# Performance work log

Measured on AMD Instinct MI355X. Metric: run time of the kernel, lower is better.

The kernel has to match this reference:

```python
import jax, jax.numpy as jnp
import numpy as np
import math

N_NODES = 4096
DEG = 32
N_EDGES = N_NODES * DEG
H = 128
NUM_NODE_STATES = 4
NUM_EDGE_STATES = 4
NUM_GRAPHS = 64
UPPER_T, LOWER_T, NUM_ITERS, TEMP_EVAL = 1.0, 0.1, 10000, 0.1
TRAINING_STEP = 1000
NEG_INF = -1.0e9


def temp_by_step(step):
    # linear anneal upper->lower over NUM_ITERS; eval temp when step == -1
    if step == -1:
        return TEMP_EVAL
    frac = min(step / float(NUM_ITERS), 1.0)
    return UPPER_T + (LOWER_T - UPPER_T) * frac


def from_binary_states(bits):
    w = 2 ** jnp.arange(bits.shape[-1], dtype=jnp.int32)
    return jnp.sum(bits.astype(jnp.int32) * w, axis=-1)


def group_argmax_onehot(vals, group, num_segments):
    # gumbel_softmax(vals, group, tau=0, use_noise=False): one-hot argmax per group
    seg_max = jax.ops.segment_max(vals, group, num_segments=num_segments)
    return (vals >= seg_max[group]).astype(jnp.int32)


def layernorm(x, g, b, eps=1e-5):
    mu = jnp.mean(x, -1, keepdims=True)
    var = jnp.mean((x - mu) ** 2, -1, keepdims=True)
    return (x - mu) * jax.lax.rsqrt(var + eps) * g + b


def select_best(emb, bits, scalars, index, num_index):
    states = 2 * from_binary_states(bits)                  # even state codes
    group = states * num_index + index.astype(jnp.int32)   # unique (state, index) id
    best = group_argmax_onehot(-scalars[:, 0], group, emb.shape[0] * num_index)
    return emb[states + best]


def _forward(node_states, edge_states, scalars, edge_index, batch_vec,
             reverse_idx, edge_pos, training_step,
             emb_virtual, emb_reciever, emb_edge, emb_static,
             w_q, w_k, w_v, w_ek, w_ev, w_comb,
             ln_q_g, ln_q_b, ln_k_g, ln_k_b,
             tg_w1, tg_b1, tg_w2, tg_b2):
    src, dst = edge_index[0], edge_index[1]
    N = node_states.shape[0]
    E = src.shape[0]
    D = E // N  # uniform in-degree (incl. self loop)
    h = w_q.shape[0]

    # per-node scalars come from the self-loop edges (exactly one per node)
    loop_vals = jnp.where((src == dst)[:, None], scalars, 0.0)
    node_scalars = jax.ops.segment_sum(loop_vals, dst, num_segments=N)  # [N,1]

    node_fts = select_best(emb_virtual, node_states, node_scalars, batch_vec, NUM_GRAPHS)
    edge_fts = emb_edge[from_binary_states(edge_states)]

    Q = layernorm(node_fts @ w_q.T, ln_q_g, ln_q_b)
    K = layernorm(node_fts @ w_k.T, ln_k_g, ln_k_b)
    V = node_fts @ w_v.T

    # combined edge K/V
    sb = select_best(emb_reciever, node_states[src], scalars, dst, N)
    sender_s = node_scalars[src]
    reciever_s = node_scalars[dst]
    rlx = (scalars < reciever_s).astype(jnp.int32)
    rlx_d = ((sender_s + scalars) < reciever_s).astype(jnp.int32)
    static_fts = emb_static[(rlx + 2 * rlx_d)[:, 0]]
    combined = jnp.concatenate([edge_fts, edge_fts[reverse_idx], static_fts], axis=-1) @ w_comb.T
    edge_K = sb @ w_ek.T
    edge_V = combined @ w_ev.T

    # dense ragged batch per destination node (to_dense_batch equivalent)
    Kc = K[src] + edge_K
    Vc = V[src] + edge_V
    dense_K = jnp.zeros((N, D, h), Kc.dtype).at[dst, edge_pos].set(Kc)
    dense_V = jnp.zeros((N, D, h), Vc.dtype).at[dst, edge_pos].set(Vc)
    mask = jnp.zeros((N, D), bool).at[dst, edge_pos].set(True)

    logits = jnp.einsum('nh,ndh->nd', Q, dense_K) / math.sqrt(h)
    logits = jnp.where(mask, logits, NEG_INF)
    thr = jax.nn.relu(node_fts @ tg_w1.T + tg_b1) @ tg_w2.T + tg_b2  # [N,1]

    tau = temp_by_step(training_step)
    diff = logits - thr
    soft_mask = jax.nn.sigmoid(diff / tau)
    if training_step == -1:
        sel = (diff >= 0).astype(logits.dtype)
    else:
        beta = min(max(tau, 0.01), 1.0)
        sm = jnp.where(mask, jax.nn.softmax(logits, axis=-1), 0.0)
        hard = (diff >= 0).astype(logits.dtype)
        proxy = (1.0 - beta) * soft_mask + beta * sm
        sel = jax.lax.stop_gradient(hard - proxy) + proxy  # straight-through
    sel = sel * mask.astype(logits.dtype)

    msg = jnp.einsum('nd,ndh->nh', sel, dense_V)  # sum aggregation (attention='hard')
    node_out = node_fts + msg
    edge_out = edge_fts + msg[dst]
    return node_out, edge_out


def _build_graph():
    # ring graph, uniform degree DEG per destination incl. self loop;
    # offsets symmetric so every edge has a reverse edge; dst-sorted.
    offs = [0]
    for k in range(1, DEG // 2):
        offs += [k, -k]
    offs.append(N_NODES // 2)  # self-reverse offset
    offs = np.asarray(offs)
    offs_mod = offs % N_NODES
    rev_t = np.array([int(np.where(offs_mod == ((-o) % N_NODES))[0][0]) for o in offs])
    t = np.tile(np.arange(DEG), N_NODES)
    dst = np.repeat(np.arange(N_NODES), DEG)
    src = (dst + offs[t]) % N_NODES
    reverse_idx = src * DEG + rev_t[t]
    return src, dst, reverse_idx, t


def setup_inputs():
    key = jax.random.key(0)
    ks = jax.random.split(key, 20)
    src, dst, reverse_idx, pos = _build_graph()
    s = 1.0 / math.sqrt(H)
    return {
        "node_states": jax.random.randint(ks[0], (N_NODES, NUM_NODE_STATES), 0, 2, dtype=jnp.int32),
        "edge_states": jax.random.randint(ks[1], (N_EDGES, NUM_EDGE_STATES), 0, 2, dtype=jnp.int32),
        "scalars": jax.random.normal(ks[2], (N_EDGES, 1), jnp.float32),
        "edge_index": jnp.asarray(np.stack([src, dst]), dtype=jnp.int32),
        "batch_vec": jnp.asarray(np.arange(N_NODES) // (N_NODES // NUM_GRAPHS), dtype=jnp.int32),
        "reverse_idx": jnp.asarray(reverse_idx, dtype=jnp.int32),
        "edge_pos": jnp.asarray(pos, dtype=jnp.int32),
        "training_step": TRAINING_STEP,
        "emb_virtual": 0.05 * jax.random.normal(ks[3], (2 ** (NUM_NODE_STATES + 1), H), jnp.float32),
        "emb_reciever": 0.05 * jax.random.normal(ks[4], (2 ** (NUM_NODE_STATES + 1), H), jnp.float32),
        "emb_edge": 0.05 * jax.random.normal(ks[5], (2 ** NUM_EDGE_STATES, H), jnp.float32),
        "emb_static": 0.05 * jax.random.normal(ks[6], (4, H), jnp.float32),
        "w_q": s * jax.random.normal(ks[7], (H, H), jnp.float32),
        "w_k": s * jax.random.normal(ks[8], (H, H), jnp.float32),
        "w_v": s * jax.random.normal(ks[9], (H, H), jnp.float32),
        "w_ek": s * jax.random.normal(ks[10], (H, H), jnp.float32),
        "w_ev": s * jax.random.normal(ks[11], (H, H), jnp.float32),
        "w_comb": s * jax.random.normal(ks[12], (H, 3 * H), jnp.float32),
        "ln_q_g": jnp.ones((H,), jnp.float32),
        "ln_q_b": jnp.zeros((H,), jnp.float32),
        "ln_k_g": jnp.ones((H,), jnp.float32),
        "ln_k_b": jnp.zeros((H,), jnp.float32),
        "tg_w1": s * jax.random.normal(ks[13], (H, H), jnp.float32),
        "tg_b1": jnp.zeros((H,), jnp.float32),
        "tg_w2": s * jax.random.normal(ks[14], (1, H), jnp.float32),
        "tg_b2": jnp.full((1,), -5.0, jnp.float32),
    }


def reference(node_states, edge_states, scalars, edge_index, batch_vec,
              reverse_idx, edge_pos, training_step,
              emb_virtual, emb_reciever, emb_edge, emb_static,
              w_q, w_k, w_v, w_ek, w_ev, w_comb,
              ln_q_g, ln_q_b, ln_k_g, ln_k_b,
              tg_w1, tg_b1, tg_w2, tg_b2):
    return _forward(node_states, edge_states, scalars, edge_index, batch_vec,
                    reverse_idx, edge_pos, training_step,
                    emb_virtual, emb_reciever, emb_edge, emb_static,
                    w_q, w_k, w_v, w_ek, w_ev, w_comb,
                    ln_q_g, ln_q_b, ln_k_g, ln_k_b,
                    tg_w1, tg_b1, tg_w2, tg_b2)
```

## Files before the change

### kernel.cpp

```cpp
#include <hip/hip_runtime.h>

#define N_NODES 4096
#define DEG 32
#define N_EDGES (N_NODES * DEG)
#define H 128
#define NUM_GRAPHS 64

#define WS_NODE_SCALARS 0
#define WS_SEG_NODE     4096
#define WS_SINT         6144
#define WS_ES           10240
#define WS_QEMB         141312
#define WS_KEMB         145408
#define WS_VEMB         149504
#define WS_EK           153600
#define WS_C1           157696
#define WS_C2           159744
#define WS_C3           161792
#define WS_EV1          162304
#define WS_EV2          164352
#define WS_EV3          166400
#define WS_QK           166912
#define WS_QEK          167936
#define WS_THR          168960

__device__ __forceinline__ unsigned int fkey(float x) {
    unsigned int u = __float_as_uint(x);
    return (u & 0x80000000u) ? ~u : (u | 0x80000000u);
}
__device__ __forceinline__ float funkey(unsigned int k) {
    unsigned int u = (k & 0x80000000u) ? (k & 0x7FFFFFFFu) : ~k;
    return __uint_as_float(u);
}
__device__ __forceinline__ int frombin4(const int* __restrict__ p) {
    int4 q = *(const int4*)p;
    return q.x + (q.y << 1) + (q.z << 2) + (q.w << 3);
}
__device__ __forceinline__ float dot128(const float* __restrict__ a, const float* __restrict__ b) {
    float s = 0.f;
#pragma unroll
    for (int k = 0; k < 128; k += 4) {
        float4 av = *(const float4*)(a + k);
        float4 bv = *(const float4*)(b + k);
        s += av.x * bv.x + av.y * bv.y + av.z * bv.z + av.w * bv.w;
    }
    return s;
}

__device__ __forceinline__ float ln256(float v, int t, const float* __restrict__ g,
                                       const float* __restrict__ bb, float* red) {
    int h = t & 127;
    red[t] = v;
    __syncthreads();
    for (int off = 64; off > 0; off >>= 1) {
        if (h < off) red[t] += red[t + off];
        __syncthreads();
    }
    float mu = red[t & 128] / 128.f;
    __syncthreads();
    float c = v - mu;
    red[t] = c * c;
    __syncthreads();
    for (int off = 64; off > 0; off >>= 1) {
        if (h < off) red[t] += red[t + off];
        __syncthreads();
    }
    float var = red[t & 128] / 128.f;
    return c * rsqrtf(var + 1e-5f) * g[h] + bb[h];
}

__global__ __launch_bounds__(256) void kA(
    const int* __restrict__ node_states, const int* __restrict__ edge_states,
    const float* __restrict__ scalars, const int* __restrict__ src,
    const int* __restrict__ dst,
    const float* __restrict__ emb_virtual, const float* __restrict__ emb_reciever,
    const float* __restrict__ emb_edge, const float* __restrict__ emb_static,
    const float* __restrict__ w_q, const float* __restrict__ w_k,
    const float* __restrict__ w_v, const float* __restrict__ w_ek,
    const float* __restrict__ w_comb,
    const float* __restrict__ ln_q_g, const float* __restrict__ ln_q_b,
    const float* __restrict__ ln_k_g, const float* __restrict__ ln_k_b,
    const float* __restrict__ tg_w1, const float* __restrict__ tg_b1,
    const float* __restrict__ tg_w2, const float* __restrict__ tg_b2,
    float* __restrict__ ws) {
    __shared__ float red[256];
    int b = blockIdx.x, t = threadIdx.x;
    unsigned int* wsu = (unsigned int*)ws;
    if (b < 98) {
        int j = 2 * b + (t >> 7), tt = t & 127;
        if (j < 32) {
            float v = dot128(emb_virtual + j * H, w_q + tt * H);
            ws[WS_QEMB + j * H + tt] = ln256(v, t, ln_q_g, ln_q_b, red);
        } else if (j < 64) {
            int s = j - 32;
            float v = dot128(emb_virtual + s * H, w_k + tt * H);
            ws[WS_KEMB + s * H + tt] = ln256(v, t, ln_k_g, ln_k_b, red);
        } else if (j < 96) {
            int s = j - 64;
            ws[WS_VEMB + s * H + tt] = dot128(emb_virtual + s * H, w_v + tt * H);
        } else if (j < 128) {
            int s = j - 96;
            ws[WS_EK + s * H + tt] = dot128(emb_reciever + s * H, w_ek + tt * H);
        } else if (j < 160) {
            int s = j - 128;
            float hval = fmaxf(dot128(emb_virtual + s * H, tg_w1 + tt * H) + tg_b1[tt], 0.f);
            red[t] = hval * tg_w2[tt];
            __syncthreads();
            for (int off = 64; off > 0; off >>= 1) {
                if (tt < off) red[t] += red[t + off];
                __syncthreads();
            }
            if (tt == 0) ws[WS_THR + s] = red[t & 128] + tg_b2[0];
        } else if (j < 176) {
            int r = j - 160;
            ws[WS_C1 + r * H + tt] = dot128(emb_edge + r * H, w_comb + tt * 384);
        } else if (j < 192) {
            int r = j - 176;
            ws[WS_C2 + r * H + tt] = dot128(emb_edge + r * H, w_comb + tt * 384 + 128);
        } else if (j < 196) {
            int r = j - 192;
            ws[WS_C3 + r * H + tt] = dot128(emb_static + r * H, w_comb + tt * 384 + 256);
        }
    } else if (b < 114) {
        __shared__ unsigned arr[64];
        int b2 = b - 98;
        int n = b2 * 256 + t;
        int si = frombin4(node_states + n * 4);
        wsu[WS_SINT + n] = (unsigned)si;
        float nsum = 0.f;
#pragma unroll 8
        for (int k = 0; k < DEG; ++k) {
            int e = n * DEG + k;
            if (src[e] == dst[e]) nsum += scalars[e];
        }
        ws[WS_NODE_SCALARS + n] = nsum;
        if (t < 64) arr[t] = 0u;
        __syncthreads();
        atomicMax(&arr[(t >> 6) * 16 + si], fkey(-nsum));
        __syncthreads();
        if (t < 64) {
            int gl = t >> 4, ssi = t & 15;
            wsu[WS_SEG_NODE + 2 * ssi * NUM_GRAPHS + (b2 * 4 + gl)] = arr[gl * 16 + ssi];
        }
    } else {
        int base = (b - 114) * 2048;
#pragma unroll
        for (int it = 0; it < 8; ++it) {
            int e = base + it * 256 + t;
            wsu[WS_ES + e] = (unsigned)frombin4(edge_states + e * 4);
        }
    }
}

__global__ __launch_bounds__(256) void kB(const float* __restrict__ w_ev,
                                          float* __restrict__ ws) {
    int b = blockIdx.x, t = threadIdx.x;
    int j = 2 * b + (t >> 7), tt = t & 127;
    if (j < 16) {
        ws[WS_EV1 + j * H + tt] = dot128(ws + WS_C1 + j * H, w_ev + tt * H);
    } else if (j < 32) {
        int r = j - 16;
        ws[WS_EV2 + r * H + tt] = dot128(ws + WS_C2 + r * H, w_ev + tt * H);
    } else if (j < 36) {
        int r = j - 32;
        ws[WS_EV3 + r * H + tt] = dot128(ws + WS_C3 + r * H, w_ev + tt * H);
    } else {
        int r = j - 36;
        if (tt < 32) {
            ws[WS_QK + r * 32 + tt] = dot128(ws + WS_QEMB + r * H, ws + WS_KEMB + tt * H);
        } else if (tt >= 64 && tt < 96) {
            int c = tt - 64;
            ws[WS_QEK + r * 32 + c] = dot128(ws + WS_QEMB + r * H, ws + WS_EK + c * H);
        }
    }
}

__global__ __launch_bounds__(256) void kC(
    const int* __restrict__ src, const int* __restrict__ batch_vec,
    const int* __restrict__ reverse_idx, const float* __restrict__ scalars,
    const int* __restrict__ training_step, const float* __restrict__ emb_virtual,
    const float* __restrict__ emb_edge, const float* __restrict__ ws,
    float* __restrict__ node_out, float* __restrict__ edge_out) {
    __shared__ float tab_v[32 * H];
    __shared__ float tab_e1[16 * H];
    __shared__ float tab_e2[16 * H];
    __shared__ float tab_e3[4 * H];
    __shared__ float tab_emb[16 * H];
    __shared__ float tab_qk[1024];
    __shared__ float tab_qek[1024];
    __shared__ float tab_thr[32];
    __shared__ float msg_sh[8 * H];
    __shared__ float sel_sh[256];
    __shared__ unsigned v_sh[256];
    __shared__ unsigned sb16[128];
    __shared__ int q_sh[8];

    const unsigned int* wsu = (const unsigned int*)ws;
    int tid = threadIdx.x, blk = blockIdx.x;

    for (int i = tid; i < 4096; i += 256) tab_v[i] = ws[WS_VEMB + i];
    for (int i = tid; i < 2048; i += 256) {
        tab_e1[i] = ws[WS_EV1 + i];
        tab_e2[i] = ws[WS_EV2 + i];
        tab_emb[i] = emb_edge[i];
    }
    for (int i = tid; i < 512; i += 256) tab_e3[i] = ws[WS_EV3 + i];
    for (int i = tid; i < 1024; i += 256) {
        tab_qk[i] = ws[WS_QK + i];
        tab_qek[i] = ws[WS_QEK + i];
    }
    if (tid < 32) tab_thr[tid] = ws[WS_THR + tid];
    if (tid < 128) sb16[tid] = 0u;
    __syncthreads();

    int g = tid >> 5, lane = tid & 31;
    int n = blk * 8 + g;
    int e = blk * 256 + tid;
    {
        int s = src[e];
        float sc = scalars[e];
        int ss = (int)wsu[WS_SINT + s], sd = (int)wsu[WS_SINT + n];
        float ns_s = ws[WS_NODE_SCALARS + s], ns_d = ws[WS_NODE_SCALARS + n];
        atomicMax(&sb16[g * 16 + ss], fkey(-sc));
        int q = 2 * sd +
                ((-ns_d >= funkey(wsu[WS_SEG_NODE + 2 * sd * NUM_GRAPHS + batch_vec[n]])) ? 1 : 0);
        int a = 2 * ss +
                ((-ns_s >= funkey(wsu[WS_SEG_NODE + 2 * ss * NUM_GRAPHS + batch_vec[s]])) ? 1 : 0);
        int rlx = (sc < ns_d) ? 1 : 0;
        int rlxd = (ns_s + sc < ns_d) ? 1 : 0;
        int st = rlx + 2 * rlxd;
        unsigned es_e = wsu[WS_ES + e];
        unsigned es_r = wsu[WS_ES + reverse_idx[e]];
        __syncthreads();
        int sbi = 2 * ss + ((-sc >= funkey(sb16[g * 16 + ss])) ? 1 : 0);
        float logit =
            (tab_qk[q * 32 + a] + tab_qek[q * 32 + sbi]) * 0.08838834764831845f;
        float thr = tab_thr[q];
        float mx = logit;
#pragma unroll
        for (int off = 16; off > 0; off >>= 1) mx = fmaxf(mx, __shfl_xor(mx, off, 32));
        float ex = __expf(logit - mx);
        float sum = ex;
#pragma unroll
        for (int off = 16; off > 0; off >>= 1) sum += __shfl_xor(sum, off, 32);
        float sm = ex / sum;
        float diff = logit - thr;
        float hard = (diff >= 0.f) ? 1.f : 0.f;
        int step = training_step[0];
        float sel;
        if (step == -1) {
            sel = hard;
        } else {
            float tau = 1.0f + (0.1f - 1.0f) * fminf((float)step / 10000.0f, 1.0f);
            float beta = fminf(fmaxf(tau, 0.01f), 1.0f);
            float soft = 1.f / (1.f + __expf(-diff / tau));
            float proxy = (1.f - beta) * soft + beta * sm;
            sel = (hard - proxy) + proxy;
        }
        sel_sh[tid] = sel;
        v_sh[tid] = (unsigned)a | (es_e << 5) | (es_r << 9) | ((unsigned)st << 13);
        if (lane == 0) q_sh[g] = q;
    }
    __syncthreads();

    {
        float4 msg = make_float4(0.f, 0.f, 0.f, 0.f);
        int vb = g * 32;
#pragma unroll 8
        for (int s2 = 0; s2 < 32; ++s2) {
            unsigned v = v_sh[vb + s2];
            float w = sel_sh[vb + s2];
            float4 rv = ((const float4*)(tab_v + (v & 31) * H))[lane];
            float4 r1 = ((const float4*)(tab_e1 + ((v >> 5) & 15) * H))[lane];
            float4 r2 = ((const float4*)(tab_e2 + ((v >> 9) & 15) * H))[lane];
            float4 r3 = ((const float4*)(tab_e3 + ((v >> 13) & 3) * H))[lane];
            msg.x += w * (rv.x + r1.x + r2.x + r3.x);
            msg.y += w * (rv.y + r1.y + r2.y + r3.y);
            msg.z += w * (rv.z + r1.z + r2.z + r3.z);
            msg.w += w * (rv.w + r1.w + r2.w + r3.w);
        }
        ((float4*)msg_sh)[tid] = msg;
        float4 ev = ((const float4*)(emb_virtual + q_sh[g] * H))[lane];
        float4 r;
        r.x = ev.x + msg.x;
        r.y = ev.y + msg.y;
        r.z = ev.z + msg.z;
        r.w = ev.w + msg.w;
        ((float4*)node_out)[n * 32 + lane] = r;
    }
    __syncthreads();

    {
        const float4* me = (const float4*)msg_sh;
        const float4* te = (const float4*)tab_emb;
        float4* eo = (float4*)edge_out;
        size_t base = (size_t)blk * 8192;
#pragma unroll
        for (int it = 0; it < 32; ++it) {
            int idx = it * 256 + tid;
            int ed = idx >> 5, p = idx & 31;
            unsigned v = v_sh[ed];
            int b4 = (v >> 5) & 15;
            float4 m = me[(ed >> 5) * 32 + p];
            float4 em = te[b4 * 32 + p];
            float4 r;
            r.x = em.x + m.x;
            r.y = em.y + m.y;
            r.z = em.z + m.z;
            r.w = em.w + m.w;
            eo[base + idx] = r;
        }
    }
}

extern "C" void kernel_launch(void* const* d_in, const int* in_sizes, int n_in,
                              void* d_out, int out_size, void* d_ws, size_t ws_size,
                              hipStream_t stream) {
    (void)in_sizes; (void)n_in; (void)out_size; (void)ws_size;
    const int* node_states = (const int*)d_in[0];
    const int* edge_states = (const int*)d_in[1];
    const float* scalars = (const float*)d_in[2];
    const int* edge_index = (const int*)d_in[3];
    const int* batch_vec = (const int*)d_in[4];
    const int* reverse_idx = (const int*)d_in[5];
    const int* training_step = (const int*)d_in[7];
    const float* emb_virtual = (const float*)d_in[8];
    const float* emb_reciever = (const float*)d_in[9];
    const float* emb_edge = (const float*)d_in[10];
    const float* emb_static = (const float*)d_in[11];
    const float* w_q = (const float*)d_in[12];
    const float* w_k = (const float*)d_in[13];
    const float* w_v = (const float*)d_in[14];
    const float* w_ek = (const float*)d_in[15];
    const float* w_ev = (const float*)d_in[16];
    const float* w_comb = (const float*)d_in[17];
    const float* ln_q_g = (const float*)d_in[18];
    const float* ln_q_b = (const float*)d_in[19];
    const float* ln_k_g = (const float*)d_in[20];
    const float* ln_k_b = (const float*)d_in[21];
    const float* tg_w1 = (const float*)d_in[22];
    const float* tg_b1 = (const float*)d_in[23];
    const float* tg_w2 = (const float*)d_in[24];
    const float* tg_b2 = (const float*)d_in[25];

    float* ws = (float*)d_ws;
    float* node_out = (float*)d_out;
    float* edge_out = node_out + (size_t)N_NODES * H;
    const int* src = edge_index;
    const int* dst = edge_index + N_EDGES;

    kA<<<178, 256, 0, stream>>>(node_states, edge_states, scalars, src, dst, emb_virtual,
                                emb_reciever, emb_edge, emb_static, w_q, w_k, w_v, w_ek,
                                w_comb, ln_q_g, ln_q_b, ln_k_g, ln_k_b, tg_w1, tg_b1,
                                tg_w2, tg_b2, ws);
    kB<<<34, 256, 0, stream>>>(w_ev, ws);
    kC<<<N_NODES / 8, 256, 0, stream>>>(src, batch_vec, reverse_idx, scalars,
                                        training_step, emb_virtual, emb_edge, ws,
                                        node_out, edge_out);
}
```

Measured before the change: 155.9 us.

## Eliminate middle kernel by fusing w_ev projection into kA and QK tables into kC

Removes the kB launch. The w_comb-then-w_ev chain is now computed inside kA through shared memory. Each kC block recomputes only the QK and QEK logit rows for its 8 destination nodes from padded K/EK tables in a single shared buffer. The aim is to drop one launch and its serialization gap, at the cost of redundant per-block dot products and an extra table load and sync phase in kC.

```diff
diff --git a/kernel.cpp b/kernel.cpp
--- a/kernel.cpp
+++ b/kernel.cpp
@@ -12,17 +12,30 @@
 #define WS_ES           10240
 #define WS_QEMB         141312
 #define WS_KEMB         145408
-#define WS_VEMB         149504
-#define WS_EK           153600
-#define WS_C1           157696
-#define WS_C2           159744
-#define WS_C3           161792
-#define WS_EV1          162304
-#define WS_EV2          164352
-#define WS_EV3          166400
-#define WS_QK           166912
-#define WS_QEK          167936
-#define WS_THR          168960
+#define WS_EK           149504
+#define WS_VEMB         153600
+#define WS_EV1          157696
+#define WS_EV2          159744
+#define WS_EV3          161792
+#define WS_THR          162304
+
+#define SM_V     0
+#define SM_E1    4096
+#define SM_E2    6144
+#define SM_E3    8192
+#define SM_EMB   8704
+#define SM_MSG   10752
+#define SM_SEL   11776
+#define SM_VSH   12032
+#define SM_SB16  12288
+#define SM_QSH   12416
+#define SM_QK8   12424
+#define SM_QEK8  12680
+#define SM_THR8  12936
+#define SM_TOTAL 12944
+#define SM_SKEMB 0
+#define SM_SEK   4224
+#define SM_SQ8   8448
 
 __device__ __forceinline__ unsigned int fkey(float x) {
     unsigned int u = __float_as_uint(x);
@@ -77,7 +90,7 @@
     const float* __restrict__ emb_edge, const float* __restrict__ emb_static,
     const float* __restrict__ w_q, const float* __restrict__ w_k,
     const float* __restrict__ w_v, const float* __restrict__ w_ek,
-    const float* __restrict__ w_comb,
+    const float* __restrict__ w_ev, const float* __restrict__ w_comb,
     const float* __restrict__ ln_q_g, const float* __restrict__ ln_q_b,
     const float* __restrict__ ln_k_g, const float* __restrict__ ln_k_b,
     const float* __restrict__ tg_w1, const float* __restrict__ tg_b1,
@@ -111,15 +124,24 @@
                 __syncthreads();
             }
             if (tt == 0) ws[WS_THR + s] = red[t & 128] + tg_b2[0];
-        } else if (j < 176) {
+        } else {
             int r = j - 160;
-            ws[WS_C1 + r * H + tt] = dot128(emb_edge + r * H, w_comb + tt * 384);
-        } else if (j < 192) {
-            int r = j - 176;
-            ws[WS_C2 + r * H + tt] = dot128(emb_edge + r * H, w_comb + tt * 384 + 128);
-        } else if (j < 196) {
-            int r = j - 192;
-            ws[WS_C3 + r * H + tt] = dot128(emb_static + r * H, w_comb + tt * 384 + 256);
+            float cv;
+            if (r < 16)
+                cv = dot128(emb_edge + r * H, w_comb + tt * 384);
+            else if (r < 32)
+                cv = dot128(emb_edge + (r - 16) * H, w_comb + tt * 384 + 128);
+            else
+                cv = dot128(emb_static + (r - 32) * H, w_comb + tt * 384 + 256);
+            red[t] = cv;
+            __syncthreads();
+            float ev = dot128(red + (t & 128), w_ev + tt * H);
+            if (r < 16)
+                ws[WS_EV1 + r * H + tt] = ev;
+            else if (r < 32)
+                ws[WS_EV2 + (r - 16) * H + tt] = ev;
+            else
+                ws[WS_EV3 + (r - 32) * H + tt] = ev;
         }
     } else if (b < 114) {
         __shared__ unsigned arr[64];
@@ -152,90 +174,88 @@
     }
 }
 
-__global__ __launch_bounds__(256) void kB(const float* __restrict__ w_ev,
-                                          float* __restrict__ ws) {
-    int b = blockIdx.x, t = threadIdx.x;
-    int j = 2 * b + (t >> 7), tt = t & 127;
-    if (j < 16) {
-        ws[WS_EV1 + j * H + tt] = dot128(ws + WS_C1 + j * H, w_ev + tt * H);
-    } else if (j < 32) {
-        int r = j - 16;
-        ws[WS_EV2 + r * H + tt] = dot128(ws + WS_C2 + r * H, w_ev + tt * H);
-    } else if (j < 36) {
-        int r = j - 32;
-        ws[WS_EV3 + r * H + tt] = dot128(ws + WS_C3 + r * H, w_ev + tt * H);
-    } else {
-        int r = j - 36;
-        if (tt < 32) {
-            ws[WS_QK + r * 32 + tt] = dot128(ws + WS_QEMB + r * H, ws + WS_KEMB + tt * H);
-        } else if (tt >= 64 && tt < 96) {
-            int c = tt - 64;
-            ws[WS_QEK + r * 32 + c] = dot128(ws + WS_QEMB + r * H, ws + WS_EK + c * H);
-        }
-    }
-}
-
 __global__ __launch_bounds__(256) void kC(
     const int* __restrict__ src, const int* __restrict__ batch_vec,
     const int* __restrict__ reverse_idx, const float* __restrict__ scalars,
     const int* __restrict__ training_step, const float* __restrict__ emb_virtual,
     const float* __restrict__ emb_edge, const float* __restrict__ ws,
     float* __restrict__ node_out, float* __restrict__ edge_out) {
-    __shared__ float tab_v[32 * H];
-    __shared__ float tab_e1[16 * H];
-    __shared__ float tab_e2[16 * H];
-    __shared__ float tab_e3[4 * H];
-    __shared__ float tab_emb[16 * H];
-    __shared__ float tab_qk[1024];
-    __shared__ float tab_qek[1024];
-    __shared__ float tab_thr[32];
-    __shared__ float msg_sh[8 * H];
-    __shared__ float sel_sh[256];
-    __shared__ unsigned v_sh[256];
-    __shared__ unsigned sb16[128];
-    __shared__ int q_sh[8];
-
+    __shared__ float sm[SM_TOTAL];
+    unsigned* smu = (unsigned*)sm;
+    int* smi = (int*)sm;
     const unsigned int* wsu = (const unsigned int*)ws;
     int tid = threadIdx.x, blk = blockIdx.x;
 
-    for (int i = tid; i < 4096; i += 256) tab_v[i] = ws[WS_VEMB + i];
-    for (int i = tid; i < 2048; i += 256) {
-        tab_e1[i] = ws[WS_EV1 + i];
-        tab_e2[i] = ws[WS_EV2 + i];
-        tab_emb[i] = emb_edge[i];
-    }
-    for (int i = tid; i < 512; i += 256) tab_e3[i] = ws[WS_EV3 + i];
+    if (tid < 128) smu[SM_SB16 + tid] = 0u;
+    for (int i = tid; i < 4096; i += 256) {
+        int r = i >> 7, c = i & 127;
+        sm[SM_SKEMB + r * 132 + c] = ws[WS_KEMB + i];
+        sm[SM_SEK + r * 132 + c] = ws[WS_EK + i];
+    }
+    if (tid < 8) {
+        int n0 = blk * 8 + tid;
+        int sd = (int)wsu[WS_SINT + n0];
+        float ns_d0 = ws[WS_NODE_SCALARS + n0];
+        int q = 2 * sd +
+                ((-ns_d0 >= funkey(wsu[WS_SEG_NODE + 2 * sd * NUM_GRAPHS + batch_vec[n0]]))
+                     ? 1
+                     : 0);
+        smi[SM_QSH + tid] = q;
+    }
+    __syncthreads();
+
     for (int i = tid; i < 1024; i += 256) {
-        tab_qk[i] = ws[WS_QK + i];
-        tab_qek[i] = ws[WS_QEK + i];
-    }
-    if (tid < 32) tab_thr[tid] = ws[WS_THR + tid];
-    if (tid < 128) sb16[tid] = 0u;
-    __syncthreads();
+        int g0 = i >> 7, c = i & 127;
+        sm[SM_SQ8 + g0 * 132 + c] = ws[WS_QEMB + smi[SM_QSH + g0] * 128 + c];
+    }
+    if (tid < 8) sm[SM_THR8 + tid] = ws[WS_THR + smi[SM_QSH + tid]];
 
     int g = tid >> 5, lane = tid & 31;
     int n = blk * 8 + g;
     int e = blk * 256 + tid;
+    int s = src[e];
+    float sc = scalars[e];
+    int ss = (int)wsu[WS_SINT + s];
+    float ns_s = ws[WS_NODE_SCALARS + s], ns_d = ws[WS_NODE_SCALARS + n];
+    atomicMax(&smu[SM_SB16 + g * 16 + ss], fkey(-sc));
+    int a = 2 * ss +
+            ((-ns_s >= funkey(wsu[WS_SEG_NODE + 2 * ss * NUM_GRAPHS + batch_vec[s]])) ? 1 : 0);
+    int st = ((sc < ns_d) ? 1 : 0) + 2 * ((ns_s + sc < ns_d) ? 1 : 0);
+    unsigned es_e = wsu[WS_ES + e];
+    unsigned es_r = wsu[WS_ES + reverse_idx[e]];
+    __syncthreads();
+
     {
-        int s = src[e];
-        float sc = scalars[e];
-        int ss = (int)wsu[WS_SINT + s], sd = (int)wsu[WS_SINT + n];
-        float ns_s = ws[WS_NODE_SCALARS + s], ns_d = ws[WS_NODE_SCALARS + n];
-        atomicMax(&sb16[g * 16 + ss], fkey(-sc));
-        int q = 2 * sd +
-                ((-ns_d >= funkey(wsu[WS_SEG_NODE + 2 * sd * NUM_GRAPHS + batch_vec[n]])) ? 1 : 0);
-        int a = 2 * ss +
-                ((-ns_s >= funkey(wsu[WS_SEG_NODE + 2 * ss * NUM_GRAPHS + batch_vec[s]])) ? 1 : 0);
-        int rlx = (sc < ns_d) ? 1 : 0;
-        int rlxd = (ns_s + sc < ns_d) ? 1 : 0;
-        int st = rlx + 2 * rlxd;
-        unsigned es_e = wsu[WS_ES + e];
-        unsigned es_r = wsu[WS_ES + reverse_idx[e]];
-        __syncthreads();
-        int sbi = 2 * ss + ((-sc >= funkey(sb16[g * 16 + ss])) ? 1 : 0);
+        int qloc = tid >> 5, c = tid & 31;
+        const float* qrow = sm + SM_SQ8 + qloc * 132;
+        const float* krow = sm + SM_SKEMB + c * 132;
+        const float* erow = sm + SM_SEK + c * 132;
+        float acc1 = 0.f, acc2 = 0.f;
+#pragma unroll
+        for (int k = 0; k < 128; k += 4) {
+            float4 qa = *(const float4*)(qrow + k);
+            float4 kb = *(const float4*)(krow + k);
+            float4 eb = *(const float4*)(erow + k);
+            acc1 += qa.x * kb.x + qa.y * kb.y + qa.z * kb.z + qa.w * kb.w;
+            acc2 += qa.x * eb.x + qa.y * eb.y + qa.z * eb.z + qa.w * eb.w;
+        }
+        sm[SM_QK8 + tid] = acc1;
+        sm[SM_QEK8 + tid] = acc2;
+    }
+    int sbi = 2 * ss + ((-sc >= funkey(smu[SM_SB16 + g * 16 + ss])) ? 1 : 0);
+    __syncthreads();
+
+    for (int i = tid; i < 4096; i += 256) sm[SM_V + i] = ws[WS_VEMB + i];
+    for (int i = tid; i < 2048; i += 256) {
+        sm[SM_E1 + i] = ws[WS_EV1 + i];
+        sm[SM_E2 + i] = ws[WS_EV2 + i];
+        sm[SM_EMB + i] = emb_edge[i];
+    }
+    for (int i = tid; i < 512; i += 256) sm[SM_E3 + i] = ws[WS_EV3 + i];
+    {
         float logit =
-            (tab_qk[q * 32 + a] + tab_qek[q * 32 + sbi]) * 0.08838834764831845f;
-        float thr = tab_thr[q];
+            (sm[SM_QK8 + g * 32 + a] + sm[SM_QEK8 + g * 32 + sbi]) * 0.08838834764831845f;
+        float thr = sm[SM_THR8 + g];
         float mx = logit;
 #pragma unroll
         for (int off = 16; off > 0; off >>= 1) mx = fmaxf(mx, __shfl_xor(mx, off, 32));
@@ -243,7 +263,7 @@
         float sum = ex;
 #pragma unroll
         for (int off = 16; off > 0; off >>= 1) sum += __shfl_xor(sum, off, 32);
-        float sm = ex / sum;
+        float sm_ = ex / sum;
         float diff = logit - thr;
         float hard = (diff >= 0.f) ? 1.f : 0.f;
         int step = training_step[0];
@@ -254,12 +274,12 @@
             float tau = 1.0f + (0.1f - 1.0f) * fminf((float)step / 10000.0f, 1.0f);
             float beta = fminf(fmaxf(tau, 0.01f), 1.0f);
             float soft = 1.f / (1.f + __expf(-diff / tau));
-            float proxy = (1.f - beta) * soft + beta * sm;
+            float proxy = (1.f - beta) * soft + beta * sm_;
             sel = (hard - proxy) + proxy;
         }
-        sel_sh[tid] = sel;
-        v_sh[tid] = (unsigned)a | (es_e << 5) | (es_r << 9) | ((unsigned)st << 13);
-        if (lane == 0) q_sh[g] = q;
+        sm[SM_SEL + tid] = sel;
+        smu[SM_VSH + tid] =
+            (unsigned)a | (es_e << 5) | (es_r << 9) | ((unsigned)st << 13);
     }
     __syncthreads();
 
@@ -268,19 +288,19 @@
         int vb = g * 32;
 #pragma unroll 8
         for (int s2 = 0; s2 < 32; ++s2) {
-            unsigned v = v_sh[vb + s2];
-            float w = sel_sh[vb + s2];
-            float4 rv = ((const float4*)(tab_v + (v & 31) * H))[lane];
-            float4 r1 = ((const float4*)(tab_e1 + ((v >> 5) & 15) * H))[lane];
-            float4 r2 = ((const float4*)(tab_e2 + ((v >> 9) & 15) * H))[lane];
-            float4 r3 = ((const float4*)(tab_e3 + ((v >> 13) & 3) * H))[lane];
+            unsigned v = smu[SM_VSH + vb + s2];
+            float w = sm[SM_SEL + vb + s2];
+            float4 rv = ((const float4*)(sm + SM_V + (v & 31) * H))[lane];
+            float4 r1 = ((const float4*)(sm + SM_E1 + ((v >> 5) & 15) * H))[lane];
+            float4 r2 = ((const float4*)(sm + SM_E2 + ((v >> 9) & 15) * H))[lane];
+            float4 r3 = ((const float4*)(sm + SM_E3 + ((v >> 13) & 3) * H))[lane];
             msg.x += w * (rv.x + r1.x + r2.x + r3.x);
             msg.y += w * (rv.y + r1.y + r2.y + r3.y);
             msg.z += w * (rv.z + r1.z + r2.z + r3.z);
             msg.w += w * (rv.w + r1.w + r2.w + r3.w);
         }
-        ((float4*)msg_sh)[tid] = msg;
-        float4 ev = ((const float4*)(emb_virtual + q_sh[g] * H))[lane];
+        ((float4*)(sm + SM_MSG))[tid] = msg;
+        float4 ev = ((const float4*)(emb_virtual + smi[SM_QSH + g] * H))[lane];
         float4 r;
         r.x = ev.x + msg.x;
         r.y = ev.y + msg.y;
@@ -291,15 +311,15 @@
     __syncthreads();
 
     {
-        const float4* me = (const float4*)msg_sh;
-        const float4* te = (const float4*)tab_emb;
+        const float4* me = (const float4*)(sm + SM_MSG);
+        const float4* te = (const float4*)(sm + SM_EMB);
         float4* eo = (float4*)edge_out;
         size_t base = (size_t)blk * 8192;
 #pragma unroll
         for (int it = 0; it < 32; ++it) {
             int idx = it * 256 + tid;
             int ed = idx >> 5, p = idx & 31;
-            unsigned v = v_sh[ed];
+            unsigned v = smu[SM_VSH + ed];
             int b4 = (v >> 5) & 15;
             float4 m = me[(ed >> 5) * 32 + p];
             float4 em = te[b4 * 32 + p];
@@ -351,9 +371,8 @@
 
     kA<<<178, 256, 0, stream>>>(node_states, edge_states, scalars, src, dst, emb_virtual,
                                 emb_reciever, emb_edge, emb_static, w_q, w_k, w_v, w_ek,
-                                w_comb, ln_q_g, ln_q_b, ln_k_g, ln_k_b, tg_w1, tg_b1,
-                                tg_w2, tg_b2, ws);
-    kB<<<34, 256, 0, stream>>>(w_ev, ws);
+                                w_ev, w_comb, ln_q_g, ln_q_b, ln_k_g, ln_k_b, tg_w1,
+                                tg_b1, tg_w2, tg_b2, ws);
     kC<<<N_NODES / 8, 256, 0, stream>>>(src, batch_vec, reverse_idx, scalars,
                                         training_step, emb_virtual, emb_edge, ws,
                                         node_out, edge_out);
```

New measurement: 152.2 us. -2.4%, faster.
